# Kernel optimization log

Measured on AMD Instinct MI355X. Metric: run time of the kernel, lower is better.

## Reference

```python
import jax, jax.numpy as jnp
import numpy as np

STRIDE = (1, 2, 2)
PADDING = ((2, 2), (3, 3), (3, 3))


def setup_inputs() -> dict:
    key = jax.random.key(0)
    kx, kw, kb = jax.random.split(key, 3)
    x = jax.random.normal(kx, (8, 3, 16, 112, 112), dtype=jnp.float32)
    weight = jax.random.normal(kw, (64, 3, 5, 7, 7), dtype=jnp.float32)
    bias = jax.random.normal(kb, (64,), dtype=jnp.float32)
    return {"x": x, "weight": weight, "bias": bias}


def reference(x, weight, bias):
    # NCDHW input, OIDHW weight -> NCDHW output; same math as the
    # torch module's explicit slice-multiply-sum conv3d.
    out = jax.lax.conv_general_dilated(
        x, weight,
        window_strides=STRIDE,
        padding=PADDING,
        dimension_numbers=("NCDHW", "OIDHW", "NCDHW"),
    )
    out = out + bias[None, :, None, None, None]
    return out
```

## Files before the change

kernel.cpp:

```cpp
#include <hip/hip_runtime.h>


typedef __attribute__((ext_vector_type(8))) short short8;
typedef __attribute__((ext_vector_type(4))) float f32x4;

#define CI 3
#define DI 16
#define HI 112
#define WI 112
#define CO 64
#define DO_ 16
#define HO 56
#define WO 56
#define HW_IN 12544
#define DHWO 50176

#define NROW 105
#define NCH 27

#define XP_ROW 144
#define XP_H   119
#define XP_D   20
#define XPAD_BYTES  (8*3*XP_D*XP_H*XP_ROW*2)
#define WBUF_OFF    XPAD_BYTES
#define WS_NEED     (WBUF_OFF + NCH*4*64*16 + 4096)

#define SEG_SH 1296
#define SEG_DW 648

__device__ __forceinline__ unsigned short f2bf(float f) {
    unsigned u = __float_as_uint(f);
    return (unsigned short)((u + 0x7FFFu + ((u >> 16) & 1u)) >> 16);
}
__device__ __forceinline__ unsigned pk_bf16(float a, float b) {
    unsigned r;
    asm("v_cvt_pk_bf16_f32 %0, %1, %2" : "=v"(r) : "v"(a), "v"(b));
    return r;
}

__device__ __forceinline__ constexpr int rb(int r) {
    const int rc = (r < NROW) ? r : (NROW - 1);
    const int c  = rc / 35;
    const int kd = (rc / 7) % 5;
    const int kh = rc % 7;
    return (c * 6 + kd) * SEG_DW + kh * (XP_ROW / 2);
}

#define XP_THREADS (8*3*XP_D*XP_H*18)
#define XP_BLOCKS  4017

__global__ void prep_all(const float* __restrict__ x, const float* __restrict__ wgt,
                         unsigned* __restrict__ xp, short8* __restrict__ wbuf) {
    if (blockIdx.x < XP_BLOCKS) {
        const int g = blockIdx.x * 256 + threadIdx.x;
        if (g >= XP_THREADS) return;
        const int s8 = g % 18;
        int r = g / 18;
        const int hp = r % XP_H; r /= XP_H;
        const int dp = r % XP_D; r /= XP_D;
        const int c  = r % 3;
        const int n  = r / 3;
        const int din = dp - 2, hin = hp - 3;
        const bool rowok = ((unsigned)din < (unsigned)DI) && ((unsigned)hin < (unsigned)HI);
        float v[8];
        const int w0 = 8 * s8 - 3;
        if (rowok && s8 >= 1 && s8 <= 13) {
            const float* xr = x + ((n * CI + c) * DI + din) * HW_IN + hin * WI + w0;
            #pragma unroll
            for (int j = 0; j < 8; ++j) v[j] = xr[j];
        } else if (rowok && (s8 == 0 || s8 == 14)) {
            const float* xr = x + ((n * CI + c) * DI + din) * HW_IN + hin * WI;
            #pragma unroll
            for (int j = 0; j < 8; ++j) {
                const int w = w0 + j;
                v[j] = ((unsigned)w < (unsigned)WI) ? xr[w] : 0.0f;
            }
        } else {
            #pragma unroll
            for (int j = 0; j < 8; ++j) v[j] = 0.0f;
        }
        uint4 o;
        o.x = pk_bf16(v[0], v[1]); o.y = pk_bf16(v[2], v[3]);
        o.z = pk_bf16(v[4], v[5]); o.w = pk_bf16(v[6], v[7]);
        *reinterpret_cast<uint4*>(xp + 4 * (size_t)g) = o;
    } else {
        const int t = (blockIdx.x - XP_BLOCKS) * 256 + threadIdx.x;
        const int lane = t & 63;
        const int cf   = t >> 6;
        const int l15  = lane & 15;
        const int kgrp = lane >> 4;
        const int co   = (cf & 3) * 16 + l15;
        const int rr   = (cf >> 2) * 4 + kgrp;
        const int rc   = (rr < NROW) ? rr : (NROW - 1);
        const int c    = rc / 35;
        const int kd   = (rc / 7) % 5;
        const int kh   = rc % 7;
        const float* wsrc = wgt + (((co * CI + c) * 5 + kd) * 7 + kh) * 7;
        short8 v;
        #pragma unroll
        for (int j = 0; j < 8; ++j) {
            float w = (rr < NROW && j < 7) ? wsrc[j] : 0.0f;
            v[j] = (short)f2bf(w);
        }
        wbuf[(size_t)cf * 64 + lane] = v;
    }
}

#define MFMA(A, B, C) __builtin_amdgcn_mfma_f32_16x16x32_bf16(A, B, C, 0, 0, 0)

__launch_bounds__(512, 4)
__global__ void conv3d_v8(const unsigned short* __restrict__ xpad,
                          const short8* __restrict__ wbuf,
                          const float* __restrict__ bias,
                          float* __restrict__ out) {
    __shared__ __align__(16) unsigned short xl[18 * SEG_SH];

    const int tid = threadIdx.x;
    int b = ((blockIdx.x & 7) * 224) + (blockIdx.x >> 3);
    const int ht  = b % 28;  b /= 28;
    const int ddp = b & 7;
    const int n   = b >> 3;
    const int ho0 = ht * 2;
    const int dd0 = ddp * 2;

    const int lane = tid & 63;
    const int wid  = tid >> 6;

    {
        const size_t nb = (size_t)(n * CI) * XP_D;
        for (int s = wid; s < 18; s += 8) {
            const int c = s / 6;
            const int p = s - c * 6;
            const char* gsrc = (const char*)(xpad +
                ((nb + (size_t)c * XP_D + (dd0 + p)) * XP_H + 2 * ho0) * XP_ROW)
                + lane * 16;
            char* ldst = (char*)&xl[s * SEG_SH];
            __builtin_amdgcn_global_load_lds(
                (const __attribute__((address_space(1))) void*)(gsrc),
                (__attribute__((address_space(3))) void*)(ldst), 16, 0, 0);
            __builtin_amdgcn_global_load_lds(
                (const __attribute__((address_space(1))) void*)(gsrc + 1024),
                (__attribute__((address_space(3))) void*)(ldst + 1024), 16, 0, 0);
            if (lane < 34)
                __builtin_amdgcn_global_load_lds(
                    (const __attribute__((address_space(1))) void*)(gsrc + 2048),
                    (__attribute__((address_space(3))) void*)(ldst + 2048), 16, 0, 0);
        }
    }
    __syncthreads();

    const int ddl  = wid & 1;
    const int hoL  = (wid >> 1) & 1;
    const int woH  = wid >> 2;
    const int l15  = lane & 15;
    const int kgrp = lane >> 4;
    const int tsp  = ddl * SEG_DW + hoL * (XP_ROW / 2) * 2 + woH * 16 + l15;

    f32x4 acc[4][2];
    #pragma unroll
    for (int a = 0; a < 4; ++a) {
        f32x4 bv;
        #pragma unroll
        for (int r = 0; r < 4; ++r) bv[r] = bias[a * 16 + kgrp * 4 + r];
        acc[a][0] = bv; acc[a][1] = bv;
    }

    const short8* wbp = wbuf + lane;
    const unsigned* xlu = reinterpret_cast<const unsigned*>(xl);

    union BxU { unsigned u[8]; short8 s[2]; };
    BxU bb[3];
    short8 Ab[3][4];

    auto tbase = [&](int ch) -> int {
        const int b0 = rb(ch * 4 + 0), b1 = rb(ch * 4 + 1);
        const int b2 = rb(ch * 4 + 2), b3 = rb(ch * 4 + 3);
        const int lo = (kgrp & 1) ? b1 : b0;
        const int hi = (kgrp & 1) ? b3 : b2;
        return ((kgrp & 2) ? hi : lo) + tsp;
    };
    auto loadA = [&](int ch, int slot) {
        #pragma unroll
        for (int a = 0; a < 4; ++a) Ab[slot][a] = wbp[(ch * 4 + a) * 64];
    };
    auto loadB = [&](int ch, int slot) {
        const unsigned* xp = xlu + tbase(ch);
        #pragma unroll
        for (int j = 0; j < 4; ++j) {
            bb[slot].u[j]     = xp[j];
            bb[slot].u[4 + j] = xp[32 + j];
        }
    };

    loadA(0, 0); loadB(0, 0);
    loadA(1, 1); loadB(1, 1);

    #pragma unroll
    for (int ch = 0; ch < NCH; ++ch) {
        const int cur = ch % 3;
        if (ch < NCH - 2) {
            const int nx = (ch + 2) % 3;
            loadA(ch + 2, nx);
            loadB(ch + 2, nx);
        }
        #pragma unroll
        for (int a = 0; a < 4; ++a) {
            acc[a][0] = MFMA(Ab[cur][a], bb[cur].s[0], acc[a][0]);
            acc[a][1] = MFMA(Ab[cur][a], bb[cur].s[1], acc[a][1]);
        }
    }

    const int dd = dd0 + ddl;
    const int ho = ho0 + hoL;
    const size_t obase = ((((size_t)n * CO) * DO_ + dd) * HO + ho) * WO;
    #pragma unroll
    for (int f = 0; f < 2; ++f) {
        const int wo = woH * 16 + f * 32 + l15;
        if (wo < WO) {
            float* op = out + obase + wo;
            #pragma unroll
            for (int a = 0; a < 4; ++a) {
                const int co = a * 16 + kgrp * 4;
                #pragma unroll
                for (int r = 0; r < 4; ++r)
                    op[(size_t)(co + r) * DHWO] = acc[a][f][r];
            }
        }
    }
}

#define FB_LR 13
#define FB_LROWS 234
#define FB_LWS 144
#define FB_XLSZ (FB_LROWS*FB_LWS)

__global__ void prep_weights_fb(const float* __restrict__ wgt, short8* __restrict__ wbuf) {
    const int t    = blockIdx.x * 64 + threadIdx.x;
    const int lane = t & 63;
    const int cf   = t >> 6;
    const int l15  = lane & 15;
    const int kgrp = lane >> 4;
    const int co   = (cf & 3) * 16 + l15;
    const int rr   = (cf >> 2) * 4 + kgrp;
    const int rc   = (rr < NROW) ? rr : (NROW - 1);
    const int c    = rc / 35;
    const int kd   = (rc / 7) % 5;
    const int kh   = rc % 7;
    const float* wsrc = wgt + (((co * CI + c) * 5 + kd) * 7 + kh) * 7;
    short8 v;
    #pragma unroll
    for (int j = 0; j < 8; ++j) {
        float w = (rr < NROW && j < 7) ? wsrc[j] : 0.0f;
        v[j] = (short)f2bf(w);
    }
    wbuf[(size_t)cf * 64 + lane] = v;
}

__launch_bounds__(512, 2)
__global__ void conv3d_mfma4(const float* __restrict__ x,
                             const short8* __restrict__ wbuf,
                             const float* __restrict__ bias,
                             float* __restrict__ out) {
    __shared__ unsigned short xl[FB_XLSZ];
    __shared__ int rowg[FB_LROWS];
    __shared__ unsigned short tabr[108];

    const int tid = threadIdx.x;
    int b = blockIdx.x;
    const int ht  = b % 14;  b /= 14;
    const int ddp = b % 8;
    const int n   = b / 8;
    const int ho0 = ht * 4;
    const int dd0 = ddp * 2;

    if (tid < FB_LROWS) {
        const int c   = tid / (6 * FB_LR);
        const int rem = tid - c * (6 * FB_LR);
        const int p   = rem / FB_LR;
        const int rl  = rem - p * FB_LR;
        const int din = dd0 - 2 + p;
        const int hin = 2 * ho0 - 3 + rl;
        const bool ok = ((unsigned)din < (unsigned)DI) && ((unsigned)hin < (unsigned)HI);
        rowg[tid] = ok ? ((n * CI + c) * DI + din) * HW_IN + hin * WI : -1;
    }
    if (tid < 108) {
        const int rc = (tid < NROW) ? tid : (NROW - 1);
        const int c  = rc / 35;
        const int kd = (rc / 7) % 5;
        const int kh = rc % 7;
        tabr[tid] = (unsigned short)(((c * 6 + kd) * FB_LR + kh) * FB_LWS);
    }
    __syncthreads();

    const int lane = tid & 63;
    const int wid  = tid >> 6;

    for (int row = wid; row < FB_LROWS; row += 8) {
        const int base = rowg[row];
        unsigned short* dst = &xl[row * FB_LWS];
        if (lane < 57) {
            float v0 = 0.0f, v1 = 0.0f;
            const int w0 = 2 * lane - 1;
            if (base >= 0) {
                if (lane >= 1)  v0 = x[base + w0];
                if (lane <= 55) v1 = x[base + w0 + 1];
            }
            *reinterpret_cast<unsigned*>(&dst[2 * lane + 2]) = pk_bf16(v0, v1);
        } else {
            const int dw = (lane == 57) ? 0 : lane;
            *reinterpret_cast<unsigned*>(&dst[2 * dw]) = 0u;
        }
    }
    __syncthreads();

    const int ddl  = wid & 1;
    const int hoL  = wid >> 1;
    const int l15  = lane & 15;
    const int kgrp = lane >> 4;
    const int woff = ddl * (FB_LR * FB_LWS) + hoL * (2 * FB_LWS);

    f32x4 acc[4][4];
    #pragma unroll
    for (int a = 0; a < 4; ++a) {
        f32x4 bv;
        #pragma unroll
        for (int r = 0; r < 4; ++r) bv[r] = bias[a * 16 + kgrp * 4 + r];
        #pragma unroll
        for (int f = 0; f < 4; ++f) acc[a][f] = bv;
    }

    const short8* wbp = wbuf + lane;
    short8 Acur[4], Anxt[4];
    #pragma unroll
    for (int a = 0; a < 4; ++a) Acur[a] = wbp[a * 64];
    int tb = (int)tabr[kgrp] + woff;

    const unsigned* xlu = reinterpret_cast<const unsigned*>(xl);

    for (int ch = 0; ch < NCH; ++ch) {
        int tbn = 0;
        if (ch + 1 < NCH) {
            tbn = (int)tabr[(ch + 1) * 4 + kgrp] + woff;
            #pragma unroll
            for (int a = 0; a < 4; ++a) Anxt[a] = wbp[((ch + 1) * 4 + a) * 64];
        }
        const unsigned* xp = xlu + (tb >> 1) + l15;
        union { unsigned u[4]; short8 s; } bx[4];
        #pragma unroll
        for (int f = 0; f < 4; ++f) {
            const unsigned* p = xp + f * 16;
            bx[f].u[0] = p[0]; bx[f].u[1] = p[1];
            bx[f].u[2] = p[2]; bx[f].u[3] = p[3];
        }
        #pragma unroll
        for (int f = 0; f < 4; ++f) {
            acc[0][f] = MFMA(Acur[0], bx[f].s, acc[0][f]);
            acc[1][f] = MFMA(Acur[1], bx[f].s, acc[1][f]);
            acc[2][f] = MFMA(Acur[2], bx[f].s, acc[2][f]);
            acc[3][f] = MFMA(Acur[3], bx[f].s, acc[3][f]);
        }
        tb = tbn;
        #pragma unroll
        for (int a = 0; a < 4; ++a) Acur[a] = Anxt[a];
    }

    const int dd = dd0 + ddl;
    const int ho = ho0 + hoL;
    #pragma unroll
    for (int f = 0; f < 4; ++f) {
        const int wo = f * 16 + l15;
        if (f < 3 || l15 < 8) {
            float* op = out + (((size_t)(n * CO) * DO_ + dd) * HO + ho) * WO + wo;
            #pragma unroll
            for (int a = 0; a < 4; ++a) {
                const int co = a * 16 + kgrp * 4;
                #pragma unroll
                for (int r = 0; r < 4; ++r)
                    op[(size_t)(co + r) * DHWO] = acc[a][f][r];
            }
        }
    }
}

extern "C" void kernel_launch(void* const* d_in, const int* in_sizes, int n_in,
                              void* d_out, int out_size, void* d_ws, size_t ws_size,
                              hipStream_t stream) {
    const float* x    = (const float*)d_in[0];
    const float* wgt  = (const float*)d_in[1];
    const float* bias = (const float*)d_in[2];
    float* out        = (float*)d_out;

    if (ws_size >= (size_t)WS_NEED) {
        unsigned* xpad = (unsigned*)d_ws;
        short8* wbuf   = (short8*)((char*)d_ws + WBUF_OFF);
        hipLaunchKernelGGL(prep_all, dim3(XP_BLOCKS + 27, 1, 1), dim3(256, 1, 1), 0,
                           stream, x, wgt, xpad, wbuf);
        hipLaunchKernelGGL(conv3d_v8, dim3(1792, 1, 1), dim3(512, 1, 1), 0, stream,
                           (const unsigned short*)xpad, wbuf, bias, out);
    } else {
        short8* wbuf = (short8*)d_ws;
        hipLaunchKernelGGL(prep_weights_fb, dim3(NCH * 4, 1, 1), dim3(64, 1, 1), 0,
                           stream, wgt, wbuf);
        hipLaunchKernelGGL(conv3d_mfma4, dim3(896, 1, 1), dim3(512, 1, 1), 0, stream,
                           x, wbuf, bias, out);
    }
}
```

Baseline: 75.46 us.

## Switch main conv kernel to 32x32x16 MFMA with 256-thread blocks

Replaces the 16x16x32 bf16 MFMA tiling with 32x32x16 MFMA tiles. Each of four waves now covers a full 64-wide output row for one (depth, height) position, and the weight buffer layout is reordered to match the 32-lane A operand. The block shrinks from 512 to 256 threads, prefetch depth drops from triple to double buffering, and sched_barriers are added around the MFMA group. The goal is fewer MFMA instructions and less LDS operand traffic per FLOP, at the cost of more accumulator registers per wave and fewer waves per block to hide latency.

```diff
diff --git a/kernel.cpp b/kernel.cpp
--- a/kernel.cpp
+++ b/kernel.cpp
@@ -1,8 +1,9 @@
 #include <hip/hip_runtime.h>
 
 
-typedef __attribute__((ext_vector_type(8))) short short8;
-typedef __attribute__((ext_vector_type(4))) float f32x4;
+typedef __attribute__((ext_vector_type(8)))  short short8;
+typedef __attribute__((ext_vector_type(4)))  float f32x4;
+typedef __attribute__((ext_vector_type(16))) float f32x16;
 
 #define CI 3
 #define DI 16
@@ -38,8 +39,8 @@
     return r;
 }
 
-__device__ __forceinline__ constexpr int rb(int r) {
-    const int rc = (r < NROW) ? r : (NROW - 1);
+__device__ __forceinline__ constexpr int rb2(int r) {
+    const int rc = (r > 104) ? 104 : r;
     const int c  = rc / 35;
     const int kd = (rc / 7) % 5;
     const int kh = rc % 7;
@@ -87,11 +88,15 @@
         const int t = (blockIdx.x - XP_BLOCKS) * 256 + threadIdx.x;
         const int lane = t & 63;
         const int cf   = t >> 6;
-        const int l15  = lane & 15;
-        const int kgrp = lane >> 4;
-        const int co   = (cf & 3) * 16 + l15;
-        const int rr   = (cf >> 2) * 4 + kgrp;
-        const int rc   = (rr < NROW) ? rr : (NROW - 1);
+        const int q    = cf & 3;
+        const int a    = q & 1;
+        const int ks   = q >> 1;
+        const int ch   = cf >> 2;
+        const int l31  = lane & 31;
+        const int hl   = lane >> 5;
+        const int co   = a * 32 + l31;
+        const int r    = ch * 4 + ks * 2 + hl;
+        const int rc   = (r > 104) ? 104 : r;
         const int c    = rc / 35;
         const int kd   = (rc / 7) % 5;
         const int kh   = rc % 7;
@@ -99,20 +104,20 @@
         short8 v;
         #pragma unroll
         for (int j = 0; j < 8; ++j) {
-            float w = (rr < NROW && j < 7) ? wsrc[j] : 0.0f;
+            float w = (r < NROW && j < 7) ? wsrc[j] : 0.0f;
             v[j] = (short)f2bf(w);
         }
         wbuf[(size_t)cf * 64 + lane] = v;
     }
 }
 
-#define MFMA(A, B, C) __builtin_amdgcn_mfma_f32_16x16x32_bf16(A, B, C, 0, 0, 0)
-
-__launch_bounds__(512, 4)
-__global__ void conv3d_v8(const unsigned short* __restrict__ xpad,
-                          const short8* __restrict__ wbuf,
-                          const float* __restrict__ bias,
-                          float* __restrict__ out) {
+#define MFMA32(A, B, C) __builtin_amdgcn_mfma_f32_32x32x16_bf16(A, B, C, 0, 0, 0)
+
+__launch_bounds__(256, 3)
+__global__ void conv3d_v10(const unsigned short* __restrict__ xpad,
+                           const short8* __restrict__ wbuf,
+                           const float* __restrict__ bias,
+                           float* __restrict__ out) {
     __shared__ __align__(16) unsigned short xl[18 * SEG_SH];
 
     const int tid = threadIdx.x;
@@ -128,7 +133,7 @@
 
     {
         const size_t nb = (size_t)(n * CI) * XP_D;
-        for (int s = wid; s < 18; s += 8) {
+        for (int s = wid; s < 18; s += 4) {
             const int c = s / 6;
             const int p = s - c * 6;
             const char* gsrc = (const char*)(xpad +
@@ -149,81 +154,88 @@
     }
     __syncthreads();
 
-    const int ddl  = wid & 1;
-    const int hoL  = (wid >> 1) & 1;
-    const int woH  = wid >> 2;
-    const int l15  = lane & 15;
-    const int kgrp = lane >> 4;
-    const int tsp  = ddl * SEG_DW + hoL * (XP_ROW / 2) * 2 + woH * 16 + l15;
-
-    f32x4 acc[4][2];
-    #pragma unroll
-    for (int a = 0; a < 4; ++a) {
-        f32x4 bv;
-        #pragma unroll
-        for (int r = 0; r < 4; ++r) bv[r] = bias[a * 16 + kgrp * 4 + r];
+    const int ddl = wid & 1;
+    const int hoL = wid >> 1;
+    const int l31 = lane & 31;
+    const int hl  = lane >> 5;
+    const int tspB = ddl * SEG_DW + hoL * 144 + l31;
+
+    f32x16 acc[2][2];
+    #pragma unroll
+    for (int a = 0; a < 2; ++a) {
+        f32x16 bv;
+        #pragma unroll
+        for (int g = 0; g < 16; ++g)
+            bv[g] = bias[a * 32 + (g & 3) + 8 * (g >> 2) + 4 * hl];
         acc[a][0] = bv; acc[a][1] = bv;
     }
 
     const short8* wbp = wbuf + lane;
     const unsigned* xlu = reinterpret_cast<const unsigned*>(xl);
 
-    union BxU { unsigned u[8]; short8 s[2]; };
-    BxU bb[3];
-    short8 Ab[3][4];
-
-    auto tbase = [&](int ch) -> int {
-        const int b0 = rb(ch * 4 + 0), b1 = rb(ch * 4 + 1);
-        const int b2 = rb(ch * 4 + 2), b3 = rb(ch * 4 + 3);
-        const int lo = (kgrp & 1) ? b1 : b0;
-        const int hi = (kgrp & 1) ? b3 : b2;
-        return ((kgrp & 2) ? hi : lo) + tsp;
-    };
+    union BxU { unsigned u[4]; short8 s; };
+    short8 As[2][4];
+    BxU    Bs[2][4];
+
     auto loadA = [&](int ch, int slot) {
         #pragma unroll
-        for (int a = 0; a < 4; ++a) Ab[slot][a] = wbp[(ch * 4 + a) * 64];
+        for (int q = 0; q < 4; ++q) As[slot][q] = wbp[(ch * 4 + q) * 64];
     };
     auto loadB = [&](int ch, int slot) {
-        const unsigned* xp = xlu + tbase(ch);
-        #pragma unroll
-        for (int j = 0; j < 4; ++j) {
-            bb[slot].u[j]     = xp[j];
-            bb[slot].u[4 + j] = xp[32 + j];
+        #pragma unroll
+        for (int ks = 0; ks < 2; ++ks) {
+            const int r0 = ch * 4 + ks * 2;
+            const int b0 = rb2(r0);
+            const int b1 = rb2(r0 + 1);
+            const int base = b0 + hl * (b1 - b0);
+            const unsigned* xp = xlu + base + tspB;
+            #pragma unroll
+            for (int f = 0; f < 2; ++f) {
+                const unsigned* p = xp + f * 32;
+                Bs[slot][ks * 2 + f].u[0] = p[0];
+                Bs[slot][ks * 2 + f].u[1] = p[1];
+                Bs[slot][ks * 2 + f].u[2] = p[2];
+                Bs[slot][ks * 2 + f].u[3] = p[3];
+            }
         }
     };
 
-    loadA(0, 0); loadB(0, 0);
-    loadA(1, 1); loadB(1, 1);
+    loadA(0, 0);
+    loadB(0, 0);
 
     #pragma unroll
     for (int ch = 0; ch < NCH; ++ch) {
-        const int cur = ch % 3;
-        if (ch < NCH - 2) {
-            const int nx = (ch + 2) % 3;
-            loadA(ch + 2, nx);
-            loadB(ch + 2, nx);
-        }
-        #pragma unroll
-        for (int a = 0; a < 4; ++a) {
-            acc[a][0] = MFMA(Ab[cur][a], bb[cur].s[0], acc[a][0]);
-            acc[a][1] = MFMA(Ab[cur][a], bb[cur].s[1], acc[a][1]);
-        }
+        if (ch + 1 < NCH) {
+            loadA(ch + 1, (ch + 1) & 1);
+            loadB(ch + 1, (ch + 1) & 1);
+        }
+        __builtin_amdgcn_sched_barrier(0);
+        const int s = ch & 1;
+        #pragma unroll
+        for (int a = 0; a < 2; ++a) {
+            #pragma unroll
+            for (int f = 0; f < 2; ++f) {
+                acc[a][f] = MFMA32(As[s][0 + a], Bs[s][0 + f].s, acc[a][f]);
+                acc[a][f] = MFMA32(As[s][2 + a], Bs[s][2 + f].s, acc[a][f]);
+            }
+        }
+        __builtin_amdgcn_sched_barrier(0);
     }
 
     const int dd = dd0 + ddl;
     const int ho = ho0 + hoL;
-    const size_t obase = ((((size_t)n * CO) * DO_ + dd) * HO + ho) * WO;
+    const size_t obase = (size_t)n * CO * DHWO + (size_t)dd * 3136 + ho * WO;
     #pragma unroll
     for (int f = 0; f < 2; ++f) {
-        const int wo = woH * 16 + f * 32 + l15;
-        if (wo < WO) {
-            float* op = out + obase + wo;
-            #pragma unroll
-            for (int a = 0; a < 4; ++a) {
-                const int co = a * 16 + kgrp * 4;
+        const int wo = f * 32 + l31;
+        if (f == 0 || l31 < 24) {
+            #pragma unroll
+            for (int a = 0; a < 2; ++a) {
                 #pragma unroll
-                for (int r = 0; r < 4; ++r)
-                    op[(size_t)(co + r) * DHWO] = acc[a][f][r];
+                for (int g = 0; g < 16; ++g) {
+                    const int co = a * 32 + (g & 3) + 8 * (g >> 2) + 4 * hl;
+                    out[obase + (size_t)co * DHWO + wo] = acc[a][f][g];
+                }
             }
         }
     }
@@ -233,6 +245,7 @@
 #define FB_LROWS 234
 #define FB_LWS 144
 #define FB_XLSZ (FB_LROWS*FB_LWS)
+#define MFMA16(A, B, C) __builtin_amdgcn_mfma_f32_16x16x32_bf16(A, B, C, 0, 0, 0)
 
 __global__ void prep_weights_fb(const float* __restrict__ wgt, short8* __restrict__ wbuf) {
     const int t    = blockIdx.x * 64 + threadIdx.x;
@@ -354,10 +367,10 @@
         }
         #pragma unroll
         for (int f = 0; f < 4; ++f) {
-            acc[0][f] = MFMA(Acur[0], bx[f].s, acc[0][f]);
-            acc[1][f] = MFMA(Acur[1], bx[f].s, acc[1][f]);
-            acc[2][f] = MFMA(Acur[2], bx[f].s, acc[2][f]);
-            acc[3][f] = MFMA(Acur[3], bx[f].s, acc[3][f]);
+            acc[0][f] = MFMA16(Acur[0], bx[f].s, acc[0][f]);
+            acc[1][f] = MFMA16(Acur[1], bx[f].s, acc[1][f]);
+            acc[2][f] = MFMA16(Acur[2], bx[f].s, acc[2][f]);
+            acc[3][f] = MFMA16(Acur[3], bx[f].s, acc[3][f]);
         }
         tb = tbn;
         #pragma unroll
@@ -395,7 +408,7 @@
         short8* wbuf   = (short8*)((char*)d_ws + WBUF_OFF);
         hipLaunchKernelGGL(prep_all, dim3(XP_BLOCKS + 27, 1, 1), dim3(256, 1, 1), 0,
                            stream, x, wgt, xpad, wbuf);
-        hipLaunchKernelGGL(conv3d_v8, dim3(1792, 1, 1), dim3(512, 1, 1), 0, stream,
+        hipLaunchKernelGGL(conv3d_v10, dim3(1792, 1, 1), dim3(256, 1, 1), 0, stream,
                            (const unsigned short*)xpad, wbuf, bias, out);
     } else {
         short8* wbuf = (short8*)d_ws;
```

Measured after the change: 67.44 us. 1.12x faster.
